# Optimization experiments

Hardware: AMD Instinct MI355X
Metric: run time of the kernel (lower is better)

## Reference

```python
import jax, jax.numpy as jnp
import numpy as np

FEATURE_SIZE = 1_000_000
FIELD_SIZE = 39
EMBED_SIZE = 32
HIDDEN = [400, 400]
BATCH = 16384


def setup_inputs() -> dict:
    key = jax.random.key(0)
    ks = jax.random.split(key, 10)
    p_emb = 1.0 / np.sqrt(FEATURE_SIZE + EMBED_SIZE)
    p_bias = 1.0 / np.sqrt(FEATURE_SIZE + 1)
    d_in = FIELD_SIZE * EMBED_SIZE
    p1 = 1.0 / np.sqrt(d_in + HIDDEN[0])
    p2 = 1.0 / np.sqrt(HIDDEN[0] + HIDDEN[1])
    d_cat = FIELD_SIZE + EMBED_SIZE + HIDDEN[-1]
    pf = 1.0 / np.sqrt(d_cat + 1)
    return {
        "feat_index": jax.random.randint(ks[0], (BATCH, FIELD_SIZE), 0, FEATURE_SIZE),
        "feat_value": jax.random.uniform(ks[1], (BATCH, FIELD_SIZE), dtype=jnp.float32),
        "feature_embedding": jax.random.uniform(ks[2], (FEATURE_SIZE, EMBED_SIZE), jnp.float32, -p_emb, p_emb),
        "feature_bias": jax.random.uniform(ks[3], (FEATURE_SIZE, 1), jnp.float32, -p_bias, p_bias),
        "W1": jax.random.uniform(ks[4], (HIDDEN[0], d_in), jnp.float32, -p1, p1),
        "b1": jnp.zeros((HIDDEN[0],), jnp.float32),
        "W2": jax.random.uniform(ks[5], (HIDDEN[1], HIDDEN[0]), jnp.float32, -p2, p2),
        "b2": jnp.zeros((HIDDEN[1],), jnp.float32),
        "final_W": jax.random.uniform(ks[6], (1, d_cat), jnp.float32, -pf, pf),
        "final_b": jnp.zeros((1,), jnp.float32),
    }


def reference(feat_index, feat_value, feature_embedding, feature_bias,
              W1, b1, W2, b2, final_W, final_b):
    B = feat_index.shape[0]
    fv = feat_value[:, :, None]                          # [B, F, 1]
    emb = feature_embedding[feat_index] * fv             # [B, F, E]

    # first-order FM term: [B, F]
    first_order = jnp.sum(feature_bias[feat_index] * fv, axis=-1)

    # second-order FM term: 0.5 * ((sum e)^2 - sum e^2), [B, E]
    sum_emb = jnp.sum(emb, axis=1)
    second_order = 0.5 * (sum_emb * sum_emb - jnp.sum(emb * emb, axis=1))

    # deep component
    deep_y = emb.reshape(B, FIELD_SIZE * EMBED_SIZE)
    deep_y = jax.nn.relu(deep_y @ W1.T + b1)
    deep_y = jax.nn.relu(deep_y @ W2.T + b2)

    concat_input = jnp.concatenate([first_order, second_order, deep_y], axis=1)
    output = concat_input @ final_W.T + final_b          # [B, 1]
    return (output, first_order, second_order, deep_y)
```

## Files before the change

### kernel.cpp

```cpp
#include <hip/hip_runtime.h>
#include <hip/hip_bf16.h>

#define BATCH 16384
#define FIELD 39
#define EMB 32
#define DIN 1248
#define K1P 1280
#define HID 400
#define K2P 448
#define NPAD 512

typedef __attribute__((ext_vector_type(8))) short short8;
typedef __attribute__((ext_vector_type(4))) float float4v;

static __device__ __forceinline__ unsigned short f2bf(float f) {
    __hip_bfloat16 h = __float2bfloat16(f);
    return *(unsigned short*)&h;
}

#define CVT_ELEMS (NPAD * K1P + NPAD * K2P + 2 * NPAD)
#define GATHER_BLOCKS (BATCH / 4)

__global__ __launch_bounds__(256) void prep_kernel(
    const int* __restrict__ feat_index,
    const float* __restrict__ feat_value,
    const float* __restrict__ emb_table,
    const float* __restrict__ bias_table,
    const float* __restrict__ W1, const float* __restrict__ b1,
    const float* __restrict__ W2, const float* __restrict__ b2,
    const float* __restrict__ fW, const float* __restrict__ fb,
    unsigned short* __restrict__ emb_ws,
    unsigned short* __restrict__ W1b,
    unsigned short* __restrict__ W2b,
    float* __restrict__ b1p, float* __restrict__ b2p,
    float* __restrict__ first_order,
    float* __restrict__ second_order,
    float* __restrict__ out0)
{
    if (blockIdx.x < GATHER_BLOCKS) {
        const int lane = threadIdx.x & 63;
        const int wave = threadIdx.x >> 6;
        const int r = blockIdx.x * 4 + wave;

        int   idx0 = 0;
        float val0 = 0.f;
        float s1 = 0.f;
        if (lane < FIELD) {
            idx0 = feat_index[r * FIELD + lane];
            val0 = feat_value[r * FIELD + lane];
            float fov = bias_table[idx0] * val0;
            first_order[r * FIELD + lane] = fov;
            s1 = fov * fW[lane];
        }

        const int fsub = lane >> 3;
        const int j4   = (lane & 7) * 4;

        float sx = 0.f, sy = 0.f, sz = 0.f, sw = 0.f;
        float qx = 0.f, qy = 0.f, qz = 0.f, qw = 0.f;

        #pragma unroll
        for (int step = 0; step < 5; ++step) {
            const int   f  = step * 8 + fsub;
            const int   fi = __shfl(idx0, f, 64);
            const float fv = __shfl(val0, f, 64);
            float4 e4 = make_float4(0.f, 0.f, 0.f, 0.f);
            if (f < FIELD) {
                float4 t = *(const float4*)(emb_table + (size_t)fi * EMB + j4);
                e4.x = t.x * fv; e4.y = t.y * fv; e4.z = t.z * fv; e4.w = t.w * fv;
                uint2 pk;
                pk.x = (unsigned)f2bf(e4.x) | ((unsigned)f2bf(e4.y) << 16);
                pk.y = (unsigned)f2bf(e4.z) | ((unsigned)f2bf(e4.w) << 16);
                *(uint2*)(emb_ws + (size_t)r * K1P + step * 256 + lane * 4) = pk;
            }
            sx += e4.x; sy += e4.y; sz += e4.z; sw += e4.w;
            qx += e4.x * e4.x; qy += e4.y * e4.y; qz += e4.z * e4.z; qw += e4.w * e4.w;
        }

        if (lane < 8) {
            uint2 z; z.x = 0u; z.y = 0u;
            *(uint2*)(emb_ws + (size_t)r * K1P + DIN + lane * 4) = z;
        }

        #pragma unroll
        for (int d = 8; d < 64; d <<= 1) {
            sx += __shfl_xor(sx, d, 64); sy += __shfl_xor(sy, d, 64);
            sz += __shfl_xor(sz, d, 64); sw += __shfl_xor(sw, d, 64);
            qx += __shfl_xor(qx, d, 64); qy += __shfl_xor(qy, d, 64);
            qz += __shfl_xor(qz, d, 64); qw += __shfl_xor(qw, d, 64);
        }

        float s2 = 0.f;
        if (lane < 8) {
            float4 so4;
            so4.x = 0.5f * (sx * sx - qx);
            so4.y = 0.5f * (sy * sy - qy);
            so4.z = 0.5f * (sz * sz - qz);
            so4.w = 0.5f * (sw * sw - qw);
            *(float4*)(second_order + (size_t)r * EMB + lane * 4) = so4;
            const float* fw = fW + FIELD + lane * 4;
            s2 = so4.x * fw[0] + so4.y * fw[1] + so4.z * fw[2] + so4.w * fw[3];
        }

        float s = s1 + s2;
        #pragma unroll
        for (int d = 1; d < 64; d <<= 1)
            s += __shfl_xor(s, d, 64);
        if (lane == 0)
            out0[r] = s + fb[0];
    } else {
        int i = (blockIdx.x - GATHER_BLOCKS) * 256 + threadIdx.x;
        const int n1p = NPAD * K1P;
        const int n2p = NPAD * K2P;
        if (i < n1p) {
            int row = i / K1P, col = i - row * K1P;
            W1b[i] = (row < HID && col < DIN)
                   ? f2bf(W1[row * DIN + col]) : (unsigned short)0;
        } else if (i < n1p + n2p) {
            int j = i - n1p;
            int row = j / K2P, col = j - row * K2P;
            W2b[j] = (row < HID && col < HID)
                   ? f2bf(W2[row * HID + col]) : (unsigned short)0;
        } else if (i < n1p + n2p + NPAD) {
            int k = i - n1p - n2p;
            b1p[k] = (k < HID) ? b1[k] : 0.f;
        } else if (i < n1p + n2p + 2 * NPAD) {
            int k = i - n1p - n2p - NPAD;
            b2p[k] = (k < HID) ? b2[k] : 0.f;
        }
    }
}

template<bool OUT_BF16, bool FINAL_DOT>
__global__ __launch_bounds__(256) void gemm_mfma(
    const unsigned short* __restrict__ A, int lda,
    const unsigned short* __restrict__ Bw, int ldb,
    const float* __restrict__ bias,
    void* __restrict__ Cp, int ldc, int stn, int K,
    const float* __restrict__ fW, float* __restrict__ out0)
{
    constexpr int BM = 128, BN = 128, BK = 64;
    __shared__ __align__(16) unsigned short As[BM * BK];
    __shared__ __align__(16) unsigned short Bs[BN * BK];
    __shared__ float part[2][BM];

    const int tid  = threadIdx.x;
    const int wave = tid >> 6;
    const int lane = tid & 63;
    const int quad = lane >> 4;
    const int l16  = lane & 15;
    const int wm = (wave & 1) * 64;
    const int wn = (wave >> 1) * 64;
    const int m0 = blockIdx.x * BM;
    const int n0 = blockIdx.y * BN;

    const int lrow8 = lane >> 3;
    const int cg    = (lane & 7) ^ lrow8;

    float4v acc[4][4];
    #pragma unroll
    for (int i = 0; i < 4; ++i)
        #pragma unroll
        for (int j = 0; j < 4; ++j)
            acc[i][j] = (float4v)(0.f);

    for (int k0 = 0; k0 < K; k0 += BK) {
        #pragma unroll
        for (int p = 0; p < 4; ++p) {
            const int seg = wave * 4 + p;
            const int r   = seg * 8 + lrow8;
            const unsigned short* gA = A + (size_t)(m0 + r) * lda + k0 + cg * 8;
            unsigned short* lA = As + seg * 512 + lane * 8;
            __builtin_amdgcn_global_load_lds(
                (const __attribute__((address_space(1))) unsigned int*)gA,
                (__attribute__((address_space(3))) unsigned int*)lA, 16, 0, 0);
            const unsigned short* gB = Bw + (size_t)(n0 + r) * ldb + k0 + cg * 8;
            unsigned short* lB = Bs + seg * 512 + lane * 8;
            __builtin_amdgcn_global_load_lds(
                (const __attribute__((address_space(1))) unsigned int*)gB,
                (__attribute__((address_space(3))) unsigned int*)lB, 16, 0, 0);
        }
        __syncthreads();

        #pragma unroll
        for (int s = 0; s < 2; ++s) {
            short8 af[4], bf[4];
            #pragma unroll
            for (int i = 0; i < 4; ++i)
                af[i] = *(const short8*)(As + (wm + i * 16 + l16) * 64
                                            + (((s * 4 + quad) ^ (l16 & 7)) * 8));
            #pragma unroll
            for (int j = 0; j < 4; ++j)
                bf[j] = *(const short8*)(Bs + (wn + j * 16 + l16) * 64
                                            + (((s * 4 + quad) ^ (l16 & 7)) * 8));
            #pragma unroll
            for (int i = 0; i < 4; ++i)
                #pragma unroll
                for (int j = 0; j < 4; ++j)
                    acc[i][j] = __builtin_amdgcn_mfma_f32_16x16x32_bf16(
                        af[i], bf[j], acc[i][j], 0, 0, 0);
        }
        __syncthreads();
    }

    #pragma unroll
    for (int i = 0; i < 4; ++i) {
        const int rbase = m0 + wm + i * 16 + quad * 4;
        #pragma unroll
        for (int j = 0; j < 4; ++j) {
            const int col = n0 + wn + j * 16 + l16;
            if (col < stn) {
                const float bv = bias[col];
                #pragma unroll
                for (int r2 = 0; r2 < 4; ++r2) {
                    float v = acc[i][j][r2] + bv;
                    v = v > 0.f ? v : 0.f;
                    acc[i][j][r2] = v;
                    if (OUT_BF16)
                        ((unsigned short*)Cp)[(size_t)(rbase + r2) * ldc + col] = f2bf(v);
                    else
                        ((float*)Cp)[(size_t)(rbase + r2) * ldc + col] = v;
                }
            } else {
                #pragma unroll
                for (int r2 = 0; r2 < 4; ++r2) acc[i][j][r2] = 0.f;
            }
        }
    }

    if (FINAL_DOT) {
        #pragma unroll
        for (int i = 0; i < 4; ++i) {
            #pragma unroll
            for (int r2 = 0; r2 < 4; ++r2) {
                float s = 0.f;
                #pragma unroll
                for (int j = 0; j < 4; ++j) {
                    const int col = n0 + wn + j * 16 + l16;
                    const float fwv = (col < HID) ? fW[FIELD + EMB + col] : 0.f;
                    s = fmaf(acc[i][j][r2], fwv, s);
                }
                s += __shfl_xor(s, 1, 64); s += __shfl_xor(s, 2, 64);
                s += __shfl_xor(s, 4, 64); s += __shfl_xor(s, 8, 64);
                if (l16 == 0)
                    part[wn >> 6][wm + i * 16 + quad * 4 + r2] = s;
            }
        }
        __syncthreads();
        if (tid < BM)
            atomicAdd(out0 + m0 + tid, part[0][tid] + part[1][tid]);
    }
}

extern "C" void kernel_launch(void* const* d_in, const int* in_sizes, int n_in,
                              void* d_out, int out_size, void* d_ws, size_t ws_size,
                              hipStream_t stream)
{
    const int*   feat_index = (const int*)d_in[0];
    const float* feat_value = (const float*)d_in[1];
    const float* emb_table  = (const float*)d_in[2];
    const float* bias_table = (const float*)d_in[3];
    const float* W1         = (const float*)d_in[4];
    const float* b1         = (const float*)d_in[5];
    const float* W2         = (const float*)d_in[6];
    const float* b2         = (const float*)d_in[7];
    const float* fW         = (const float*)d_in[8];
    const float* fb         = (const float*)d_in[9];

    float* out = (float*)d_out;
    float* out0 = out;
    float* fo   = out + BATCH;
    float* so   = out + (size_t)BATCH * (1 + FIELD);
    float* dy   = out + (size_t)BATCH * (1 + FIELD + EMB);

    unsigned short* emb_ws = (unsigned short*)d_ws;
    unsigned short* h1     = emb_ws + (size_t)BATCH * K1P;
    unsigned short* W1b    = h1 + (size_t)BATCH * K2P;
    unsigned short* W2b    = W1b + (size_t)NPAD * K1P;
    float*          b1p    = (float*)(W2b + (size_t)NPAD * K2P);
    float*          b2p    = b1p + NPAD;

    const int cvt_blocks = (CVT_ELEMS + 255) / 256;
    prep_kernel<<<GATHER_BLOCKS + cvt_blocks, 256, 0, stream>>>(
        feat_index, feat_value, emb_table, bias_table,
        W1, b1, W2, b2, fW, fb,
        emb_ws, W1b, W2b, b1p, b2p, fo, so, out0);

    dim3 grid_g(BATCH / 128, NPAD / 128);
    gemm_mfma<true, false><<<grid_g, 256, 0, stream>>>(
        emb_ws, K1P, W1b, K1P, b1p, h1, K2P, K2P, K1P, nullptr, nullptr);
    gemm_mfma<false, true><<<grid_g, 256, 0, stream>>>(
        h1, K2P, W2b, K2P, b2p, dy, HID, HID, K2P, fW, out0);
}
```

Before: 267.3 us.

## Template GEMM K-tile, skip dead padded waves, use nontemporal output stores

```diff
diff --git a/kernel.cpp b/kernel.cpp
--- a/kernel.cpp
+++ b/kernel.cpp
@@ -131,7 +131,7 @@
     }
 }
 
-template<bool OUT_BF16, bool FINAL_DOT>
+template<int BK, bool OUT_BF16, bool FINAL_DOT>
 __global__ __launch_bounds__(256) void gemm_mfma(
     const unsigned short* __restrict__ A, int lda,
     const unsigned short* __restrict__ Bw, int ldb,
@@ -139,7 +139,10 @@
     void* __restrict__ Cp, int ldc, int stn, int K,
     const float* __restrict__ fW, float* __restrict__ out0)
 {
-    constexpr int BM = 128, BN = 128, BK = 64;
+    constexpr int BM = 128, BN = 128;
+    constexpr int CH  = BK / 8;
+    constexpr int RPS = 512 / BK;
+    constexpr int PASSES = BM * BK / 2048;
     __shared__ __align__(16) unsigned short As[BM * BK];
     __shared__ __align__(16) unsigned short Bs[BN * BK];
     __shared__ float part[2][BM];
@@ -154,8 +157,10 @@
     const int m0 = blockIdx.x * BM;
     const int n0 = blockIdx.y * BN;
 
-    const int lrow8 = lane >> 3;
-    const int cg    = (lane & 7) ^ lrow8;
+    const int lr   = lane / CH;
+    const int slot = lane % CH;
+
+    const bool waveDead = (wave >= 2) && (n0 + 64 >= stn);
 
     float4v acc[4][4];
     #pragma unroll
@@ -166,39 +171,44 @@
 
     for (int k0 = 0; k0 < K; k0 += BK) {
         #pragma unroll
-        for (int p = 0; p < 4; ++p) {
-            const int seg = wave * 4 + p;
-            const int r   = seg * 8 + lrow8;
-            const unsigned short* gA = A + (size_t)(m0 + r) * lda + k0 + cg * 8;
+        for (int p = 0; p < PASSES; ++p) {
+            const int seg = wave * PASSES + p;
+            const int r   = seg * RPS + lr;
+            const int c   = slot ^ (r & (CH - 1));
+            const unsigned short* gA = A + (size_t)(m0 + r) * lda + k0 + c * 8;
             unsigned short* lA = As + seg * 512 + lane * 8;
             __builtin_amdgcn_global_load_lds(
                 (const __attribute__((address_space(1))) unsigned int*)gA,
                 (__attribute__((address_space(3))) unsigned int*)lA, 16, 0, 0);
-            const unsigned short* gB = Bw + (size_t)(n0 + r) * ldb + k0 + cg * 8;
-            unsigned short* lB = Bs + seg * 512 + lane * 8;
-            __builtin_amdgcn_global_load_lds(
-                (const __attribute__((address_space(1))) unsigned int*)gB,
-                (__attribute__((address_space(3))) unsigned int*)lB, 16, 0, 0);
+            if (!waveDead) {
+                const unsigned short* gB = Bw + (size_t)(n0 + r) * ldb + k0 + c * 8;
+                unsigned short* lB = Bs + seg * 512 + lane * 8;
+                __builtin_amdgcn_global_load_lds(
+                    (const __attribute__((address_space(1))) unsigned int*)gB,
+                    (__attribute__((address_space(3))) unsigned int*)lB, 16, 0, 0);
+            }
         }
         __syncthreads();
 
-        #pragma unroll
-        for (int s = 0; s < 2; ++s) {
-            short8 af[4], bf[4];
+        if (!waveDead) {
             #pragma unroll
-            for (int i = 0; i < 4; ++i)
-                af[i] = *(const short8*)(As + (wm + i * 16 + l16) * 64
-                                            + (((s * 4 + quad) ^ (l16 & 7)) * 8));
-            #pragma unroll
-            for (int j = 0; j < 4; ++j)
-                bf[j] = *(const short8*)(Bs + (wn + j * 16 + l16) * 64
-                                            + (((s * 4 + quad) ^ (l16 & 7)) * 8));
-            #pragma unroll
-            for (int i = 0; i < 4; ++i)
+            for (int s = 0; s < BK / 32; ++s) {
+                short8 af[4], bf[4];
+                #pragma unroll
+                for (int i = 0; i < 4; ++i)
+                    af[i] = *(const short8*)(As + (wm + i * 16 + l16) * BK
+                                            + (((s * 4 + quad) ^ (l16 & (CH - 1))) * 8));
                 #pragma unroll
                 for (int j = 0; j < 4; ++j)
-                    acc[i][j] = __builtin_amdgcn_mfma_f32_16x16x32_bf16(
-                        af[i], bf[j], acc[i][j], 0, 0, 0);
+                    bf[j] = *(const short8*)(Bs + (wn + j * 16 + l16) * BK
+                                            + (((s * 4 + quad) ^ (l16 & (CH - 1))) * 8));
+                #pragma unroll
+                for (int i = 0; i < 4; ++i)
+                    #pragma unroll
+                    for (int j = 0; j < 4; ++j)
+                        acc[i][j] = __builtin_amdgcn_mfma_f32_16x16x32_bf16(
+                            af[i], bf[j], acc[i][j], 0, 0, 0);
+            }
         }
         __syncthreads();
     }
@@ -219,7 +229,8 @@
                     if (OUT_BF16)
                         ((unsigned short*)Cp)[(size_t)(rbase + r2) * ldc + col] = f2bf(v);
                     else
-                        ((float*)Cp)[(size_t)(rbase + r2) * ldc + col] = v;
+                        __builtin_nontemporal_store(
+                            v, ((float*)Cp) + (size_t)(rbase + r2) * ldc + col);
                 }
             } else {
                 #pragma unroll
@@ -287,8 +298,8 @@
         emb_ws, W1b, W2b, b1p, b2p, fo, so, out0);
 
     dim3 grid_g(BATCH / 128, NPAD / 128);
-    gemm_mfma<true, false><<<grid_g, 256, 0, stream>>>(
+    gemm_mfma<128, true, false><<<grid_g, 256, 0, stream>>>(
         emb_ws, K1P, W1b, K1P, b1p, h1, K2P, K2P, K1P, nullptr, nullptr);
-    gemm_mfma<false, true><<<grid_g, 256, 0, stream>>>(
+    gemm_mfma<64, false, true><<<grid_g, 256, 0, stream>>>(
         h1, K2P, W2b, K2P, b2p, dy, HID, HID, K2P, fW, out0);
 }
```

Measured after the change: 264.0 us. About the same (-1.2%).
